# Performance work log

Measured on AMD Instinct MI355X. Metric: run time of the kernel, lower is better.

The kernel has to match this reference:

```python
import jax, jax.numpy as jnp
import numpy as np

B, T, TEMP_IN, STAT_IN = 8, 512, 32, 16
TEMP_H, STAT_H, ATTN_H, N_LAYERS, N_CLS = 64, 32, 32, 2, 2
BN_INV = float(1.0 / np.sqrt(1.0 + 1e-5))  # eval-mode BN, running_mean=0, running_var=1


def _bn(x, g, b):
    return x * (g * BN_INV) + b


def _lrelu(x):
    return jax.nn.leaky_relu(x, 0.01)


def _mlp_layer(x, W, b, g, beta):
    return _lrelu(_bn(x @ W + b, g, beta))


def setup_inputs() -> dict:
    key = jax.random.key(0)
    ks = jax.random.split(key, 32)
    lengths = jax.random.randint(ks[0], (B,), T // 2, T + 1)
    mask_q = jnp.arange(T)[None, :] < lengths[:, None]          # [B,T]
    masks = mask_q[:, :, None]                                   # [B,T,1] bool
    x_temp = jax.random.normal(ks[1], (B, T, TEMP_IN), jnp.float32) * mask_q[..., None]
    x_stat = jax.random.normal(ks[2], (B, STAT_IN), jnp.float32)
    t = jnp.sort(jax.random.uniform(ks[3], (B, T), jnp.float32) * 100.0, axis=-1)
    p = lambda k, sh, s=0.1: jax.random.normal(k, sh, jnp.float32) * s
    inp = dict(x_temp=x_temp, x_stat=x_stat, t=t, masks=masks, lengths=lengths)
    # attn_mlp: Linear(1,H)+BN+LeakyReLU, Linear(H,1)
    inp['aw0'] = p(ks[4], (1, ATTN_H), 0.5); inp['ab0'] = p(ks[5], (ATTN_H,))
    inp['ag'] = 1.0 + p(ks[6], (ATTN_H,)); inp['abeta'] = p(ks[7], (ATTN_H,))
    inp['aw1'] = p(ks[8], (ATTN_H, 1), 0.2); inp['ab1'] = p(ks[9], (1,))
    # top non_linear_temp / non_linear_stat
    inp['tw'] = p(ks[10], (TEMP_IN, TEMP_H)); inp['tb'] = p(ks[11], (TEMP_H,))
    inp['tg'] = 1.0 + p(ks[12], (TEMP_H,)); inp['tbeta'] = p(ks[13], (TEMP_H,))
    inp['sw'] = p(ks[14], (STAT_IN, STAT_H)); inp['sb'] = p(ks[15], (STAT_H,))
    inp['sg'] = 1.0 + p(ks[16], (STAT_H,)); inp['sbeta'] = p(ks[17], (STAT_H,))
    # stacked SimtaPlusLayer params [L,...]
    inp['lw_t'] = p(ks[18], (N_LAYERS, TEMP_H + STAT_H, TEMP_H))
    inp['lb_t'] = p(ks[19], (N_LAYERS, TEMP_H))
    inp['lg_t'] = 1.0 + p(ks[20], (N_LAYERS, TEMP_H)); inp['lbeta_t'] = p(ks[21], (N_LAYERS, TEMP_H))
    inp['lw_s'] = p(ks[22], (N_LAYERS, STAT_H, STAT_H))
    inp['lb_s'] = p(ks[23], (N_LAYERS, STAT_H))
    inp['lg_s'] = 1.0 + p(ks[24], (N_LAYERS, STAT_H)); inp['lbeta_s'] = p(ks[25], (N_LAYERS, STAT_H))
    inp['cw'] = p(ks[26], (TEMP_H + STAT_H, N_CLS)); inp['cb'] = p(ks[27], (N_CLS,))
    return inp


def _forward(x_temp, x_stat, t, aw0, ab0, ag, abeta, aw1, ab1, tw, tb, tg, tbeta,
             sw, sb, sg, sbeta, lw_t, lb_t, lg_t, lbeta_t, lw_s, lb_s, lg_s, lbeta_s,
             cw, cb, mask_q):
    # dt[b,i,j] = (t[b,j]-t[b,i]) / (max dt + eps)
    dt = t[:, None, :] - t[:, :, None]
    dt = dt / (dt.max() + 1e-8)
    # pairwise-MLP temporal attention: [B,T,T,H] intermediate (memory-bound)
    h = _lrelu(_bn(dt[..., None] * aw0[0] + ab0, ag, abeta))
    a = (h @ aw1)[..., 0] + ab1[0]                                # [B,T,T]
    temp_attn = jax.nn.softmax(jnp.where(mask_q[:, None, :], a, -9e8), axis=-1)

    x_t = _mlp_layer(x_temp, tw, tb, tg, tbeta)                   # [B,T,Ct]
    x_s = _mlp_layer(x_stat, sw, sb, sg, sbeta)                   # [B,Cs]

    for l in range(lw_t.shape[0]):
        xs_rep = jnp.broadcast_to(x_s[:, None, :], (x_t.shape[0], x_t.shape[1], x_s.shape[-1]))
        x = _mlp_layer(jnp.concatenate([x_t, xs_rep], axis=-1), lw_t[l], lb_t[l], lg_t[l], lbeta_t[l])
        x = x * mask_q[..., None]                                 # pad_packed zeros invalid rows
        d = jnp.asarray(x.shape[-1], x.dtype)
        qk = jnp.einsum('bic,bjc->bij', x, x) / jnp.sqrt(d)
        self_attn = jax.nn.softmax(qk, axis=-1)                   # torch softmaxes over all keys (pads give qk=0)
        attn = (self_attn + temp_attn) * mask_q[:, None, :]       # masked_fill(~mask, 0) on key columns
        x_s = _mlp_layer(x_s, lw_s[l], lb_s[l], lg_s[l], lbeta_s[l])
        x_t = (attn @ x) * mask_q[..., None]

    xs_rep = jnp.broadcast_to(x_s[:, None, :], (x_t.shape[0], x_t.shape[1], x_s.shape[-1]))
    output = jnp.concatenate([x_t, xs_rep], axis=-1) @ cw + cb    # [B,T,C]
    output = output * mask_q[..., None]
    # per-segment argmax over (logit1 - logit0), gather that row
    diff = jnp.where(mask_q, output[..., 1] - output[..., 0], -1e30)
    idx = jnp.argmax(diff, axis=1)                                # [B]
    output_max = output[jnp.arange(output.shape[0]), idx]         # [B,C]
    return output, output_max


def reference(x_temp, x_stat, t, masks, lengths, aw0, ab0, ag, abeta, aw1, ab1,
              tw, tb, tg, tbeta, sw, sb, sg, sbeta,
              lw_t, lb_t, lg_t, lbeta_t, lw_s, lb_s, lg_s, lbeta_s, cw, cb):
    mask_q = jnp.any(masks, axis=-1)                              # [B,T]
    return _forward(x_temp, x_stat, t, aw0, ab0, ag, abeta, aw1, ab1, tw, tb, tg, tbeta,
                    sw, sb, sg, sbeta, lw_t, lb_t, lg_t, lbeta_t, lw_s, lb_s, lg_s, lbeta_s,
                    cw, cb, mask_q)
```

## Files before the change

### kernel.cpp

```cpp
#include <hip/hip_runtime.h>

#define B 8
#define T 512
#define TEMP_IN 32
#define STAT_IN 16
#define TEMP_H 64
#define STAT_H 32
#define ATTN_H 32
#define N_CLS 2
#define BN_INV 0.99999500003749969f
#define R 8

struct KP {
    const float *x_temp, *x_stat, *t;
    const int* lengths;
    const float *aw0, *ab0, *ag, *abeta, *aw1, *ab1;
    const float *tw, *tb, *tg, *tbeta;
    const float *sw, *sb, *sg, *sbeta;
    const float *lw_t, *lb_t, *lg_t, *lbeta_t;
    const float *lw_s, *lb_s, *lg_s, *lbeta_s;
    const float *cw, *cb;
    float *XL, *XL2;
    unsigned long long* cand;
    unsigned *f1, *f2;
    unsigned *arr;
    float *out, *outmax;
};

__device__ __forceinline__ float lrelu(float x) {
    return fmaxf(x, 0.f) + 0.01f * fminf(x, 0.f);
}
__device__ __forceinline__ float wave_max(float x) {
    #pragma unroll
    for (int o = 32; o > 0; o >>= 1) x = fmaxf(x, __shfl_xor(x, o));
    return x;
}
__device__ __forceinline__ float wave_sum(float x) {
    #pragma unroll
    for (int o = 32; o > 0; o >>= 1) x += __shfl_xor(x, o);
    return x;
}
__device__ __forceinline__ unsigned ordf(float f) {
    unsigned u = __float_as_uint(f);
    return (u & 0x80000000u) ? ~u : (u | 0x80000000u);
}

__device__ __forceinline__ void stg_llc(float* p, float v) {
    __hip_atomic_store(p, v, __ATOMIC_RELAXED, __HIP_MEMORY_SCOPE_AGENT);
}
__device__ __forceinline__ float ldg_llc(const float* p) {
    return __hip_atomic_load(p, __ATOMIC_RELAXED, __HIP_MEMORY_SCOPE_AGENT);
}
__device__ __forceinline__ void drain_vm() {
    asm volatile("s_waitcnt vmcnt(0)" ::: "memory");
}
__device__ __forceinline__ void fence_acq_wg() {
    __builtin_amdgcn_fence(__ATOMIC_ACQUIRE, "workgroup");
}

struct Shm {
    float att[R][T];
    float part[4][R][TEMP_H];
    float xi[R][TEMP_H];
    float x1[R][TEMP_H];
    float t_s[T];
    float s_w[3 * ATTN_H + 1];
    float xs[3][STAT_H];
    float xr[4][TEMP_IN];
    float h0s[4][TEMP_H + STAT_H];
    float o_rc[R][2];
    int lastf;
};

__device__ __forceinline__ void publish(unsigned* f) {
    drain_vm();
    __syncthreads();
    if (threadIdx.x == 0)
        __hip_atomic_store(f, 1u, __ATOMIC_RELAXED, __HIP_MEMORY_SCOPE_AGENT);
}
__device__ __forceinline__ void wait_batch(const unsigned* fbase, int tid) {
    if (tid < 64) {
        const unsigned* p = fbase + tid * 16;
        while (__hip_atomic_load(p, __ATOMIC_RELAXED, __HIP_MEMORY_SCOPE_AGENT) == 0u)
            __builtin_amdgcn_s_sleep(4);
    }
    __syncthreads();
    fence_acq_wg();
}

__device__ __forceinline__ void front(const KP& P, Shm& S, int b, int i0, int len,
                                      int lane, int wave) {
    #pragma unroll
    for (int p = 0; p < 2; ++p) {
        int r = p * 4 + wave;
        int i = i0 + r;
        int row = b * T + i;
        if (lane < TEMP_IN) S.xr[wave][lane] = P.x_temp[row * TEMP_IN + lane];
        __syncthreads();
        float acc = P.tb[lane];
        #pragma unroll
        for (int k = 0; k < TEMP_IN; ++k) acc += S.xr[wave][k] * P.tw[k * TEMP_H + lane];
        acc = acc * (P.tg[lane] * BN_INV) + P.tbeta[lane];
        S.h0s[wave][lane] = lrelu(acc);
        if (lane < STAT_H) S.h0s[wave][TEMP_H + lane] = S.xs[0][lane];
        __syncthreads();
        float a2 = P.lb_t[lane];
        #pragma unroll
        for (int k = 0; k < TEMP_H + STAT_H; ++k) a2 += S.h0s[wave][k] * P.lw_t[k * TEMP_H + lane];
        a2 = a2 * (P.lg_t[lane] * BN_INV) + P.lbeta_t[lane];
        a2 = lrelu(a2);
        stg_llc(&P.XL[(size_t)row * TEMP_H + lane], (i < len) ? a2 : 0.f);
        __syncthreads();
    }
}

__device__ __forceinline__ void temp_compute(Shm& S, float tmpv[2][8], float inv_dt,
                                             int i0, int len, int lane, int wave) {
    float ab1v = S.s_w[3 * ATTN_H];
    #pragma unroll
    for (int rr = 0; rr < 2; ++rr) {
        int r = wave + rr * 4;
        float ti = S.t_s[i0 + r];
        float a[8], dtq[8];
        #pragma unroll
        for (int q = 0; q < 8; ++q) {
            dtq[q] = (S.t_s[lane + q * 64] - ti) * inv_dt;
            a[q] = ab1v;
        }
        #pragma unroll 4
        for (int k = 0; k < ATTN_H; ++k) {
            float Wk = S.s_w[k];
            float Ck = S.s_w[ATTN_H + k];
            float w1k = S.s_w[2 * ATTN_H + k];
            #pragma unroll
            for (int q = 0; q < 8; ++q) {
                float h = dtq[q] * Wk + Ck;
                h = fmaxf(h, 0.f) + 0.01f * fminf(h, 0.f);
                a[q] += h * w1k;
            }
        }
        float m2 = -1e30f;
        #pragma unroll
        for (int q = 0; q < 8; ++q) {
            int j = lane + q * 64;
            a[q] = (j < len) ? a[q] : -9e8f;
            m2 = fmaxf(m2, a[q]);
        }
        m2 = wave_max(m2);
        float s2 = 0.f;
        #pragma unroll
        for (int q = 0; q < 8; ++q) { a[q] = expf(a[q] - m2); s2 += a[q]; }
        s2 = wave_sum(s2);
        float inv2 = 1.0f / s2;
        #pragma unroll
        for (int q = 0; q < 8; ++q) tmpv[rr][q] = a[q] * inv2;
    }
}

template <int EPI>
__device__ __forceinline__ void attn_core(const KP& P, Shm& S, const float* src,
                                          const float tmpv[2][8],
                                          int b, int i0, int len, int tid, int lane, int wave,
                                          int tile) {
    for (int idx = tid; idx < R * TEMP_H; idx += 256)
        S.xi[idx >> 6][idx & 63] = src[((size_t)(b * T + i0 + (idx >> 6))) * TEMP_H + (idx & 63)];
    __syncthreads();
    for (int j = tid; j < T; j += 256) {
        const float4* xj4 = reinterpret_cast<const float4*>(&src[((size_t)(b * T + j)) * TEMP_H]);
        float acc[R];
        #pragma unroll
        for (int r = 0; r < R; ++r) acc[r] = 0.f;
        #pragma unroll
        for (int c4 = 0; c4 < TEMP_H / 4; ++c4) {
            float4 xv = xj4[c4];
            #pragma unroll
            for (int r = 0; r < R; ++r) {
                acc[r] += S.xi[r][c4 * 4 + 0] * xv.x;
                acc[r] += S.xi[r][c4 * 4 + 1] * xv.y;
                acc[r] += S.xi[r][c4 * 4 + 2] * xv.z;
                acc[r] += S.xi[r][c4 * 4 + 3] * xv.w;
            }
        }
        #pragma unroll
        for (int r = 0; r < R; ++r) S.att[r][j] = acc[r] * 0.125f;
    }
    __syncthreads();
    #pragma unroll
    for (int rr = 0; rr < 2; ++rr) {
        int r = wave + rr * 4;
        float v[8];
        float m = -1e30f;
        #pragma unroll
        for (int q = 0; q < 8; ++q) { v[q] = S.att[r][lane + q * 64]; m = fmaxf(m, v[q]); }
        m = wave_max(m);
        float s = 0.f;
        #pragma unroll
        for (int q = 0; q < 8; ++q) { v[q] = expf(v[q] - m); s += v[q]; }
        s = wave_sum(s);
        float invs = 1.0f / s;
        #pragma unroll
        for (int q = 0; q < 8; ++q) {
            int j = lane + q * 64;
            S.att[r][j] = (j < len) ? (v[q] * invs + tmpv[rr][q]) : 0.f;
        }
    }
    __syncthreads();
    float acc2[R];
    #pragma unroll
    for (int r = 0; r < R; ++r) acc2[r] = 0.f;
    for (int j = wave * 128; j < wave * 128 + 128; ++j) {
        float xv = src[((size_t)(b * T + j)) * TEMP_H + lane];
        #pragma unroll
        for (int r = 0; r < R; ++r) acc2[r] += S.att[r][j] * xv;
    }
    #pragma unroll
    for (int r = 0; r < R; ++r) S.part[wave][r][lane] = acc2[r];
    __syncthreads();
    for (int idx = tid; idx < R * TEMP_H; idx += 256) {
        int r = idx >> 6, cc = idx & 63;
        float sum = S.part[0][r][cc] + S.part[1][r][cc] + S.part[2][r][cc] + S.part[3][r][cc];
        S.x1[r][cc] = ((i0 + r) < len) ? sum : 0.f;
    }
    __syncthreads();

    if (EPI == 0) {
        const float* lw1    = P.lw_t + (TEMP_H + STAT_H) * TEMP_H;
        const float* lb1    = P.lb_t + TEMP_H;
        const float* lg1    = P.lg_t + TEMP_H;
        const float* lbeta1 = P.lbeta_t + TEMP_H;
        #pragma unroll
        for (int rr = 0; rr < 2; ++rr) {
            int r = wave * 2 + rr;
            int i = i0 + r;
            float acc = lb1[lane];
            #pragma unroll
            for (int k = 0; k < TEMP_H; ++k) acc += S.x1[r][k] * lw1[k * TEMP_H + lane];
            #pragma unroll
            for (int k = 0; k < STAT_H; ++k) acc += S.xs[1][k] * lw1[(TEMP_H + k) * TEMP_H + lane];
            acc = acc * (lg1[lane] * BN_INV) + lbeta1[lane];
            acc = lrelu(acc);
            stg_llc(&P.XL2[((size_t)(b * T + i)) * TEMP_H + lane], (i < len) ? acc : 0.f);
        }
    } else {
        if (tid < R * N_CLS) {
            int r = tid >> 1, cls = tid & 1;
            int i = i0 + r;
            float o = P.cb[cls];
            #pragma unroll
            for (int k = 0; k < TEMP_H; ++k) o += S.x1[r][k] * P.cw[k * N_CLS + cls];
            #pragma unroll
            for (int k = 0; k < STAT_H; ++k) o += S.xs[2][k] * P.cw[(TEMP_H + k) * N_CLS + cls];
            if (i >= len) o = 0.f;
            stg_llc(&P.out[((size_t)(b * T + i)) * N_CLS + cls], o);
            S.o_rc[r][cls] = o;
        }
        __syncthreads();
        if (tid == 0) {
            float best = -3e30f; int bi = i0;
            for (int r = 0; r < R; ++r) {
                int i = i0 + r;
                float diff = (i < len) ? (S.o_rc[r][1] - S.o_rc[r][0]) : -1e30f;
                if (diff > best) { best = diff; bi = i; }
            }
            unsigned long long pack =
                ((unsigned long long)ordf(best) << 32) | (unsigned)(~(unsigned)bi);
            __hip_atomic_store(&P.cand[(b * 64 + tile) * 8], pack,
                               __ATOMIC_RELAXED, __HIP_MEMORY_SCOPE_AGENT);
            drain_vm();
            unsigned old = __hip_atomic_fetch_add(&P.arr[b * 16], 1u,
                                                  __ATOMIC_RELAXED, __HIP_MEMORY_SCOPE_AGENT);
            S.lastf = (old == 63u) ? 1 : 0;
        }
        __syncthreads();
        if (S.lastf) {
            fence_acq_wg();
            if (tid < 64) {
                unsigned long long c = __hip_atomic_load(&P.cand[(b * 64 + tid) * 8],
                                                         __ATOMIC_RELAXED, __HIP_MEMORY_SCOPE_AGENT);
                #pragma unroll
                for (int o = 32; o > 0; o >>= 1) {
                    unsigned long long oc = __shfl_xor(c, o);
                    c = (oc > c) ? oc : c;
                }
                if (tid == 0) {
                    int idx = (int)(~(unsigned)(c & 0xffffffffu));
                    float o0 = ldg_llc(&P.out[((size_t)(b * T + idx)) * N_CLS + 0]);
                    float o1 = ldg_llc(&P.out[((size_t)(b * T + idx)) * N_CLS + 1]);
                    stg_llc(&P.outmax[b * 2 + 0], o0);
                    stg_llc(&P.outmax[b * 2 + 1], o1);
                }
            }
        }
    }
}

template <int PHASE>
__global__ void __launch_bounds__(256, 2) k_run(KP P) {
    __shared__ Shm S;
    int tid = threadIdx.x, lane = tid & 63, wave = tid >> 6;
    int blk = blockIdx.x;
    int b = blk & 7, tile = blk >> 3, i0 = tile * R;
    int len = P.lengths[b];
    float tmpv[2][8];

    if (tid < STAT_H) {
        float acc = P.sb[tid];
        #pragma unroll
        for (int k = 0; k < STAT_IN; ++k) acc += P.x_stat[b * STAT_IN + k] * P.sw[k * STAT_H + tid];
        acc = acc * (P.sg[tid] * BN_INV) + P.sbeta[tid];
        S.xs[0][tid] = lrelu(acc);
    }
    __syncthreads();

    if (PHASE == 0 || PHASE == 3) front(P, S, b, i0, len, lane, wave);
    if (PHASE == 3) publish(&P.f1[(b * 64 + tile) * 16]);

    if (PHASE != 0) {
        if (tid < ATTN_H) {
            float g = P.ag[tid] * BN_INV;
            S.s_w[tid]              = P.aw0[tid] * g;
            S.s_w[ATTN_H + tid]     = P.ab0[tid] * g + P.abeta[tid];
            S.s_w[2 * ATTN_H + tid] = P.aw1[tid];
        }
        if (tid == 0) S.s_w[3 * ATTN_H] = P.ab1[0];
        S.t_s[tid] = P.t[b * T + tid];
        S.t_s[tid + 256] = P.t[b * T + tid + 256];
        float d = P.t[(lane & 7) * T + (T - 1)] - P.t[(lane & 7) * T];
        d = wave_max(d);
        float inv_dt = 1.0f / (d + 1e-8f);
        __syncthreads();
        if (tid < STAT_H) {
            float a2 = P.lb_s[tid];
            #pragma unroll
            for (int k = 0; k < STAT_H; ++k) a2 += S.xs[0][k] * P.lw_s[k * STAT_H + tid];
            a2 = a2 * (P.lg_s[tid] * BN_INV) + P.lbeta_s[tid];
            S.xs[1][tid] = lrelu(a2);
        }
        __syncthreads();
        if (tid < STAT_H) {
            float a2 = P.lb_s[STAT_H + tid];
            #pragma unroll
            for (int k = 0; k < STAT_H; ++k) a2 += S.xs[1][k] * P.lw_s[(STAT_H + k) * STAT_H + tid];
            a2 = a2 * (P.lg_s[STAT_H + tid] * BN_INV) + P.lbeta_s[STAT_H + tid];
            S.xs[2][tid] = lrelu(a2);
        }
        __syncthreads();
        temp_compute(S, tmpv, inv_dt, i0, len, lane, wave);
        __syncthreads();
    }

    if (PHASE == 3) wait_batch(P.f1 + b * 64 * 16, tid);
    if (PHASE == 1 || PHASE == 3)
        attn_core<0>(P, S, P.XL, tmpv, b, i0, len, tid, lane, wave, tile);
    if (PHASE == 3) {
        publish(&P.f2[(b * 64 + tile) * 16]);
        wait_batch(P.f2 + b * 64 * 16, tid);
    }
    if (PHASE == 2 || PHASE == 3)
        attn_core<1>(P, S, P.XL2, tmpv, b, i0, len, tid, lane, wave, tile);
}

extern "C" void kernel_launch(void* const* d_in, const int* in_sizes, int n_in,
                              void* d_out, int out_size, void* d_ws, size_t ws_size,
                              hipStream_t stream) {
    KP p;
    p.x_temp  = (const float*)d_in[0];
    p.x_stat  = (const float*)d_in[1];
    p.t       = (const float*)d_in[2];
    p.lengths = (const int*)d_in[4];
    p.aw0 = (const float*)d_in[5];
    p.ab0 = (const float*)d_in[6];
    p.ag  = (const float*)d_in[7];
    p.abeta = (const float*)d_in[8];
    p.aw1 = (const float*)d_in[9];
    p.ab1 = (const float*)d_in[10];
    p.tw  = (const float*)d_in[11];
    p.tb  = (const float*)d_in[12];
    p.tg  = (const float*)d_in[13];
    p.tbeta = (const float*)d_in[14];
    p.sw  = (const float*)d_in[15];
    p.sb  = (const float*)d_in[16];
    p.sg  = (const float*)d_in[17];
    p.sbeta = (const float*)d_in[18];
    p.lw_t = (const float*)d_in[19];
    p.lb_t = (const float*)d_in[20];
    p.lg_t = (const float*)d_in[21];
    p.lbeta_t = (const float*)d_in[22];
    p.lw_s = (const float*)d_in[23];
    p.lb_s = (const float*)d_in[24];
    p.lg_s = (const float*)d_in[25];
    p.lbeta_s = (const float*)d_in[26];
    p.cw = (const float*)d_in[27];
    p.cb = (const float*)d_in[28];

    float* ws = (float*)d_ws;
    p.XL  = ws;
    p.XL2 = ws + (size_t)B * T * TEMP_H;
    p.cand = (unsigned long long*)(ws + 2 * (size_t)B * T * TEMP_H);
    p.f1  = (unsigned*)(p.cand + B * 64 * 8);
    p.f2  = p.f1 + B * 64 * 16;
    p.arr = p.f2 + B * 64 * 16;
    p.out = (float*)d_out;
    p.outmax = p.out + (size_t)B * T * N_CLS;

    size_t flagbytes = (size_t)B * 64 * 8 * 8 + 2 * (size_t)B * 64 * 16 * 4 + (size_t)B * 16 * 4;
    hipMemsetAsync(p.cand, 0, flagbytes, stream);

    void* args[] = { (void*)&p };
    hipError_t err = hipLaunchCooperativeKernel((const void*)k_run<3>, dim3(B * (T / R)),
                                                dim3(256), args, 0, stream);
    if (err != hipSuccess) {
        (void)hipGetLastError();
        k_run<0><<<B * (T / R), 256, 0, stream>>>(p);
        k_run<1><<<B * (T / R), 256, 0, stream>>>(p);
        k_run<2><<<B * (T / R), 256, 0, stream>>>(p);
    }
}
```

Measured before the change: 102.8 us.

## Reuse layer-output rows from LDS, vectorize LDS reads, use fast exp and lrelu

In the fused persistent path, each block now keeps its own layer-1 outputs in LDS and skips reloading those rows from global memory for the second attention layer. The QK and AV inner loops read LDS as float4, and the AV loop loads four rows per step to add memory-level parallelism. expf is replaced by __expf, and leaky ReLU becomes a single fmax. Together these cut global traffic and instruction count, at the cost of slightly lower exp precision.

```diff
diff --git a/kernel.cpp b/kernel.cpp
--- a/kernel.cpp
+++ b/kernel.cpp
@@ -28,7 +28,7 @@
 };
 
 __device__ __forceinline__ float lrelu(float x) {
-    return fmaxf(x, 0.f) + 0.01f * fminf(x, 0.f);
+    return fmaxf(x, 0.01f * x);
 }
 __device__ __forceinline__ float wave_max(float x) {
     #pragma unroll
@@ -135,7 +135,7 @@
             #pragma unroll
             for (int q = 0; q < 8; ++q) {
                 float h = dtq[q] * Wk + Ck;
-                h = fmaxf(h, 0.f) + 0.01f * fminf(h, 0.f);
+                h = fmaxf(h, 0.01f * h);
                 a[q] += h * w1k;
             }
         }
@@ -149,7 +149,7 @@
         m2 = wave_max(m2);
         float s2 = 0.f;
         #pragma unroll
-        for (int q = 0; q < 8; ++q) { a[q] = expf(a[q] - m2); s2 += a[q]; }
+        for (int q = 0; q < 8; ++q) { a[q] = __expf(a[q] - m2); s2 += a[q]; }
         s2 = wave_sum(s2);
         float inv2 = 1.0f / s2;
         #pragma unroll
@@ -157,13 +157,15 @@
     }
 }
 
-template <int EPI>
+template <int EPI, bool LOAD_XI>
 __device__ __forceinline__ void attn_core(const KP& P, Shm& S, const float* src,
                                           const float tmpv[2][8],
                                           int b, int i0, int len, int tid, int lane, int wave,
                                           int tile) {
-    for (int idx = tid; idx < R * TEMP_H; idx += 256)
-        S.xi[idx >> 6][idx & 63] = src[((size_t)(b * T + i0 + (idx >> 6))) * TEMP_H + (idx & 63)];
+    if (LOAD_XI) {
+        for (int idx = tid; idx < R * TEMP_H; idx += 256)
+            S.xi[idx >> 6][idx & 63] = src[((size_t)(b * T + i0 + (idx >> 6))) * TEMP_H + (idx & 63)];
+    }
     __syncthreads();
     for (int j = tid; j < T; j += 256) {
         const float4* xj4 = reinterpret_cast<const float4*>(&src[((size_t)(b * T + j)) * TEMP_H]);
@@ -175,10 +177,8 @@
             float4 xv = xj4[c4];
             #pragma unroll
             for (int r = 0; r < R; ++r) {
-                acc[r] += S.xi[r][c4 * 4 + 0] * xv.x;
-                acc[r] += S.xi[r][c4 * 4 + 1] * xv.y;
-                acc[r] += S.xi[r][c4 * 4 + 2] * xv.z;
-                acc[r] += S.xi[r][c4 * 4 + 3] * xv.w;
+                float4 xi4 = *reinterpret_cast<const float4*>(&S.xi[r][c4 * 4]);
+                acc[r] += xi4.x * xv.x + xi4.y * xv.y + xi4.z * xv.z + xi4.w * xv.w;
             }
         }
         #pragma unroll
@@ -195,7 +195,7 @@
         m = wave_max(m);
         float s = 0.f;
         #pragma unroll
-        for (int q = 0; q < 8; ++q) { v[q] = expf(v[q] - m); s += v[q]; }
+        for (int q = 0; q < 8; ++q) { v[q] = __expf(v[q] - m); s += v[q]; }
         s = wave_sum(s);
         float invs = 1.0f / s;
         #pragma unroll
@@ -208,10 +208,21 @@
     float acc2[R];
     #pragma unroll
     for (int r = 0; r < R; ++r) acc2[r] = 0.f;
-    for (int j = wave * 128; j < wave * 128 + 128; ++j) {
-        float xv = src[((size_t)(b * T + j)) * TEMP_H + lane];
-        #pragma unroll
-        for (int r = 0; r < R; ++r) acc2[r] += S.att[r][j] * xv;
+    {
+        const float* srow = src + (size_t)b * T * TEMP_H + lane;
+        int j0 = wave * 128;
+        for (int g = 0; g < 32; ++g) {
+            int j = j0 + g * 4;
+            float xv0 = srow[(size_t)(j + 0) * TEMP_H];
+            float xv1 = srow[(size_t)(j + 1) * TEMP_H];
+            float xv2 = srow[(size_t)(j + 2) * TEMP_H];
+            float xv3 = srow[(size_t)(j + 3) * TEMP_H];
+            #pragma unroll
+            for (int r = 0; r < R; ++r) {
+                float4 a4 = *reinterpret_cast<const float4*>(&S.att[r][j]);
+                acc2[r] += a4.x * xv0 + a4.y * xv1 + a4.z * xv2 + a4.w * xv3;
+            }
+        }
     }
     #pragma unroll
     for (int r = 0; r < R; ++r) S.part[wave][r][lane] = acc2[r];
@@ -239,7 +250,9 @@
             for (int k = 0; k < STAT_H; ++k) acc += S.xs[1][k] * lw1[(TEMP_H + k) * TEMP_H + lane];
             acc = acc * (lg1[lane] * BN_INV) + lbeta1[lane];
             acc = lrelu(acc);
-            stg_llc(&P.XL2[((size_t)(b * T + i)) * TEMP_H + lane], (i < len) ? acc : 0.f);
+            float vout = (i < len) ? acc : 0.f;
+            stg_llc(&P.XL2[((size_t)(b * T + i)) * TEMP_H + lane], vout);
+            S.xi[r][lane] = vout;
         }
     } else {
         if (tid < R * N_CLS) {
@@ -351,13 +364,14 @@
 
     if (PHASE == 3) wait_batch(P.f1 + b * 64 * 16, tid);
     if (PHASE == 1 || PHASE == 3)
-        attn_core<0>(P, S, P.XL, tmpv, b, i0, len, tid, lane, wave, tile);
+        attn_core<0, true>(P, S, P.XL, tmpv, b, i0, len, tid, lane, wave, tile);
     if (PHASE == 3) {
         publish(&P.f2[(b * 64 + tile) * 16]);
         wait_batch(P.f2 + b * 64 * 16, tid);
-    }
-    if (PHASE == 2 || PHASE == 3)
-        attn_core<1>(P, S, P.XL2, tmpv, b, i0, len, tid, lane, wave, tile);
+        attn_core<1, false>(P, S, P.XL2, tmpv, b, i0, len, tid, lane, wave, tile);
+    } else if (PHASE == 2) {
+        attn_core<1, true>(P, S, P.XL2, tmpv, b, i0, len, tid, lane, wave, tile);
+    }
 }
 
 extern "C" void kernel_launch(void* const* d_in, const int* in_sizes, int n_in,
```

Result: no change. 103.4 us (+0.6%).
